# Performance work log

Measured on AMD Instinct MI355X. Metric: run time of the kernel, lower is better.

Reference implementation:

```python
import jax, jax.numpy as jnp
import numpy as np

B, D, H = 4096, 64, 512  # batch, event dim, MLP hidden


def _net(z, t, W1, b1, W2, b2, W3, b3):
    # z: [..., D]; t: scalar, broadcast as a time feature column
    tcol = jnp.broadcast_to(t, z.shape[:-1] + (1,))
    x = jnp.concatenate([z, tcol], axis=-1)            # [..., D+1]
    h = jnp.tanh(x @ W1 + b1)                          # [..., H]
    h = jnp.tanh(h @ W2 + b2)                          # [..., H]
    return h @ W3 + b3                                 # [..., D]


def setup_inputs() -> dict:
    key = jax.random.key(0)
    ks = jax.random.split(key, 6)
    s_in = 1.0 / np.sqrt(D + 1)
    s_h = 1.0 / np.sqrt(H)
    return {
        "z": jax.random.normal(ks[0], (B, D), dtype=jnp.float32),
        "log_pz": jnp.zeros((B, 1), dtype=jnp.float32),
        "t": jax.random.uniform(ks[1], (1,), dtype=jnp.float32),
        "W1": jax.random.normal(ks[2], (D + 1, H), dtype=jnp.float32) * s_in,
        "b1": jnp.zeros((H,), dtype=jnp.float32),
        "W2": jax.random.normal(ks[3], (H, H), dtype=jnp.float32) * s_h,
        "b2": jnp.zeros((H,), dtype=jnp.float32),
        "W3": jax.random.normal(ks[4], (H, D), dtype=jnp.float32) * s_h,
        "b3": jnp.zeros((D,), dtype=jnp.float32),
    }


def reference(z, log_pz, t, W1, b1, W2, b2, W3, b3):
    tval = t[0]
    # velocity field v = net(z, t), batched
    v = _net(z, tval, W1, b1, W2, b2, W3, b3)          # [B, D]
    # exact Jacobian trace: replaces the torch per-dim autograd.grad loop
    # with a fully vectorized per-sample forward-mode Jacobian.
    f_single = lambda zi: _net(zi, tval, W1, b1, W2, b2, W3, b3)  # [D] -> [D]
    jac = jax.vmap(jax.jacfwd(f_single))(z)            # [B, D, D]
    dlogp_dt = -jnp.trace(jac, axis1=1, axis2=2)[:, None]  # [B, 1]
    return (v, dlogp_dt)
```

## Files before the change

### kernel.cpp

```cpp
#include <hip/hip_runtime.h>
#include <hip/hip_bf16.h>

#define BB 4096
#define DD 64
#define HH 512

typedef short short8 __attribute__((ext_vector_type(8)));
typedef float f32x4  __attribute__((ext_vector_type(4)));
typedef __hip_bfloat16 bf16;

__device__ __forceinline__ float tanh_fast(float x) {
    float e = __expf(2.0f * x);
    return 1.0f - __fdividef(2.0f, 1.0f + e);
}

__device__ __forceinline__ void st_swz(bf16* base, int row, int col, int rs, float v) {
    base[row * rs + ((((col >> 3) ^ (row & 7))) << 3) + (col & 7)] = __float2bfloat16(v);
}

#define GLD1(dst, addr)                                                      \
  asm volatile("global_load_dwordx4 %0, %1, off" : "=&v"(dst) : "v"(addr))

#define GLD2(e0, e1, addr)                                                   \
  asm volatile("global_load_dwordx4 %0, %2, off\n\t"                         \
               "global_load_dwordx4 %1, %2, off offset:1024"                 \
               : "=&v"(e0), "=&v"(e1) : "v"(addr))

#define GLD4(e0, e1, e2, e3, addr)                                           \
  asm volatile("global_load_dwordx4 %0, %4, off\n\t"                         \
               "global_load_dwordx4 %1, %4, off offset:1024\n\t"             \
               "global_load_dwordx4 %2, %4, off offset:2048\n\t"             \
               "global_load_dwordx4 %3, %4, off offset:3072"                 \
               : "=&v"(e0), "=&v"(e1), "=&v"(e2), "=&v"(e3) : "v"(addr))

#define WAITV(n)                                                             \
  do { asm volatile("s_waitcnt vmcnt(" #n ")" ::: "memory");                 \
       __builtin_amdgcn_sched_barrier(0); } while (0)

#define LGKMBAR()                                                            \
  do { asm volatile("s_waitcnt lgkmcnt(0)" ::: "memory");                    \
       __builtin_amdgcn_s_barrier();                                         \
       __builtin_amdgcn_sched_barrier(0); } while (0)

__global__ __launch_bounds__(256) void prep_kernel(
    const float* __restrict__ t, const float* __restrict__ W1,
    const float* __restrict__ b1, const float* __restrict__ W2,
    const float* __restrict__ W3, const float* __restrict__ b3,
    bf16* __restrict__ W1p, bf16* __restrict__ W2p, bf16* __restrict__ W3p,
    bf16* __restrict__ Pp, float* __restrict__ b1eff, float* __restrict__ out)
{
    const int tid  = threadIdx.x;
    const int bx   = blockIdx.x;
    const int lane = tid & 63;
    const int r    = lane & 15;
    const int kq   = lane >> 4;

    if (bx < 160) {
        int T = bx * 4 + (tid >> 6);
        const float* src;
        bf16* dst;
        int stride;
        if (T < 64) {
            int w = T >> 2, s = (T >> 1) & 1, f = T & 1;
            src = W1 + (size_t)(s * 32 + kq * 8) * HH + (w * 2 + f) * 16 + r;
            stride = HH;
            dst = W1p + (size_t)T * 512 + lane * 8;
        } else if (T < 576) {
            int tt = T - 64;
            int cw = tt >> 4, s = tt & 15;
            src = W2 + (size_t)(s * 32 + kq * 8) * HH + cw * 16 + r;
            stride = HH;
            dst = W2p + (size_t)tt * 512 + lane * 8;
        } else {
            int tt = T - 576;
            int q = tt >> 2, f = tt & 3;
            src = W3 + (size_t)(q * 32 + kq * 8) * DD + f * 16 + r;
            stride = DD;
            dst = W3p + (size_t)tt * 512 + lane * 8;
        }
        short8 v;
#pragma unroll
        for (int j = 0; j < 8; ++j)
            v[j] = (short)__bfloat16_as_ushort(__float2bfloat16(src[(size_t)j * stride]));
        *(short8*)dst = v;
    } else if (bx < 288) {
        int pt = (bx - 160) * 4 + (tid >> 6);
        int cw = pt >> 4, s = pt & 15;
        int k  = cw * 16 + r;
        int j0 = s * 32 + kq * 8;
        float acc[8] = {};
        const float* w3row = W3 + (size_t)k * DD;
        for (int d = 0; d < DD; ++d) {
            float w3 = w3row[d];
            const float4* w1p4 = (const float4*)(W1 + (size_t)d * HH + j0);
            float4 x = w1p4[0], y = w1p4[1];
            acc[0] += x.x * w3; acc[1] += x.y * w3;
            acc[2] += x.z * w3; acc[3] += x.w * w3;
            acc[4] += y.x * w3; acc[5] += y.y * w3;
            acc[6] += y.z * w3; acc[7] += y.w * w3;
        }
        short8 v;
#pragma unroll
        for (int j = 0; j < 8; ++j)
            v[j] = (short)__bfloat16_as_ushort(
                __float2bfloat16(acc[j] * W2[(size_t)(j0 + j) * HH + k]));
        *(short8*)(Pp + (size_t)pt * 512 + lane * 8) = v;
    } else if (bx == 288) {
        float tv = t[0];
        b1eff[tid]       = b1[tid]       + tv * W1[(size_t)64 * HH + tid];
        b1eff[tid + 256] = b1[tid + 256] + tv * W1[(size_t)64 * HH + tid + 256];
    } else {
        int idx = (bx - 289) * 1024 + tid * 4;
        if (idx < BB * DD) {
            int col = idx & 63;
            *(float4*)(out + idx) =
                make_float4(b3[col], b3[col + 1], b3[col + 2], b3[col + 3]);
        } else {
            *(float4*)(out + idx) = make_float4(0.f, 0.f, 0.f, 0.f);
        }
    }
}

__global__ __launch_bounds__(1024, 2) void fused_rows(
    const float* __restrict__ z, const bf16* __restrict__ W1p,
    const bf16* __restrict__ W2p, const bf16* __restrict__ W3p,
    const bf16* __restrict__ Pp, const float* __restrict__ b1eff,
    const float* __restrict__ b2,
    float* __restrict__ outV, float* __restrict__ outTr)
{
    __shared__ alignas(16) char smem[88064];
    bf16* zt   = (bf16*)smem;
    bf16* h1   = (bf16*)(smem + 4096);
    bf16* at   = (bf16*)(smem + 36864);
    bf16* h2   = (bf16*)(smem + 69632);
    float* trp = (float*)(smem + 86016);
    float* vp  = (float*)smem;

    const int tid  = threadIdx.x;
    const int wid  = tid >> 6;
    const int lane = tid & 63;
    const int r    = lane & 15;
    const int kq   = lane >> 4;
    const int rx   = r & 7;
    const int laneE = lane * 8;
    const int rt   = blockIdx.x >> 1;
    const int ch   = blockIdx.x & 1;
    const int bm   = rt * 32;

    float bias1[2];
#pragma unroll
    for (int f = 0; f < 2; ++f) bias1[f] = b1eff[wid * 32 + f * 16 + r];
    float bias2 = b2[ch * 256 + wid * 16 + r];
    asm volatile("" :: "v"(bias1[0]), "v"(bias1[1]), "v"(bias2));

    {
        int i = tid * 2;
        int row = i >> 6, col = i & 63;
        float2 v = *(const float2*)(z + (size_t)(bm + row) * DD + col);
        st_swz(zt, row, col,     64, v.x);
        st_swz(zt, row, col + 1, 64, v.y);
    }

    short8 q0, q1, q2, q3, p0, p1;
    const bf16* Wb1 = W1p + (size_t)wid * 2048 + laneE;
    GLD2(q0, q1, Wb1);
    GLD2(p0, p1, Wb1 + 1024);
    LGKMBAR();

    f32x4 acc1[2][2] = {};
    WAITV(2);
#pragma unroll
    for (int g = 0; g < 2; ++g) {
        short8 av = *(const short8*)(zt + (g * 16 + r) * 64 + ((kq ^ rx) << 3));
        acc1[g][0] = __builtin_amdgcn_mfma_f32_16x16x32_bf16(av, q0, acc1[g][0], 0, 0, 0);
        acc1[g][1] = __builtin_amdgcn_mfma_f32_16x16x32_bf16(av, q1, acc1[g][1], 0, 0, 0);
    }
    WAITV(0);
#pragma unroll
    for (int g = 0; g < 2; ++g) {
        short8 av = *(const short8*)(zt + (g * 16 + r) * 64 + (((4 + kq) ^ rx) << 3));
        acc1[g][0] = __builtin_amdgcn_mfma_f32_16x16x32_bf16(av, p0, acc1[g][0], 0, 0, 0);
        acc1[g][1] = __builtin_amdgcn_mfma_f32_16x16x32_bf16(av, p1, acc1[g][1], 0, 0, 0);
    }
    short8 rbW[4], rbP[4];
    const bf16* Wb2 = W2p + (size_t)(ch * 16 + wid) * 8192 + laneE;
    const bf16* WbE = Pp  + (size_t)(ch * 16 + wid) * 8192 + laneE;
    GLD1(rbW[0], Wb2);        GLD1(rbP[0], WbE);
    GLD1(rbW[1], Wb2 + 512);  GLD1(rbP[1], WbE + 512);
    GLD1(rbW[2], Wb2 + 1024); GLD1(rbP[2], WbE + 1024);
#pragma unroll
    for (int g = 0; g < 2; ++g)
#pragma unroll
        for (int f = 0; f < 2; ++f) {
            int col = wid * 32 + f * 16 + r;
#pragma unroll
            for (int v = 0; v < 4; ++v) {
                int row = g * 16 + kq * 4 + v;
                float h = tanh_fast(acc1[g][f][v] + bias1[f]);
                st_swz(h1, row, col, 512, h);
                st_swz(at, row, col, 512, fmaf(-h, h, 1.0f));
            }
        }
    LGKMBAR();

    f32x4 acc2[2] = {};
    f32x4 accE[2] = {};
#pragma unroll
    for (int s = 0; s < 16; ++s) {
        int co = (((s * 4 + kq) ^ rx) << 3);
        short8 a1v[2], aav[2];
#pragma unroll
        for (int g = 0; g < 2; ++g) {
            a1v[g] = *(const short8*)(h1 + (g * 16 + r) * 512 + co);
            aav[g] = *(const short8*)(at + (g * 16 + r) * 512 + co);
        }
        if (s + 3 < 16) {
            GLD1(rbW[(s + 3) & 3], Wb2 + (s + 3) * 512);
            GLD1(rbP[(s + 3) & 3], WbE + (s + 3) * 512);
            WAITV(6);
        } else if (s + 2 < 16) { WAITV(4); }
        else if (s + 1 < 16)   { WAITV(2); }
        else                   { WAITV(0); }
#pragma unroll
        for (int g = 0; g < 2; ++g) {
            acc2[g] = __builtin_amdgcn_mfma_f32_16x16x32_bf16(a1v[g], rbW[s & 3], acc2[g], 0, 0, 0);
            accE[g] = __builtin_amdgcn_mfma_f32_16x16x32_bf16(aav[g], rbP[s & 3], accE[g], 0, 0, 0);
        }
    }
    f32x4 bsq[2];
    {
        int colL = wid * 16 + r;
#pragma unroll
        for (int g = 0; g < 2; ++g)
#pragma unroll
            for (int v = 0; v < 4; ++v) {
                int row = g * 16 + kq * 4 + v;
                float h = tanh_fast(acc2[g][v] + bias2);
                st_swz(h2, row, colL, 256, h);
                bsq[g][v] = fmaf(-h, h, 1.0f);
            }
        const int kw = wid & 7;
        const bf16* Wb3 = W3p + (size_t)(ch * 8 + kw) * 2048 + laneE;
        GLD4(q0, q1, q2, q3, Wb3);
#pragma unroll
        for (int g = 0; g < 2; ++g)
#pragma unroll
            for (int v = 0; v < 4; ++v) {
                float p = accE[g][v] * bsq[g][v];
                p += __shfl_xor(p, 1);
                p += __shfl_xor(p, 2);
                p += __shfl_xor(p, 4);
                p += __shfl_xor(p, 8);
                if (r == 0) trp[wid * 32 + g * 16 + kq * 4 + v] = p;
            }
    }
    LGKMBAR();

    {
        const int kw = wid & 7, rp = wid >> 3;
        f32x4 c0 = {}, c1 = {}, c2 = {}, c3 = {};
        short8 av = *(const short8*)(h2 + (rp * 16 + r) * 256 + (((kw * 4 + kq) ^ rx) << 3));
        WAITV(0);
        c0 = __builtin_amdgcn_mfma_f32_16x16x32_bf16(av, q0, c0, 0, 0, 0);
        c1 = __builtin_amdgcn_mfma_f32_16x16x32_bf16(av, q1, c1, 0, 0, 0);
        c2 = __builtin_amdgcn_mfma_f32_16x16x32_bf16(av, q2, c2, 0, 0, 0);
        c3 = __builtin_amdgcn_mfma_f32_16x16x32_bf16(av, q3, c3, 0, 0, 0);
#pragma unroll
        for (int v = 0; v < 4; ++v) {
            int row = rp * 16 + kq * 4 + v;
            vp[kw * 2048 + row * 64 + 0 * 16 + r] = c0[v];
            vp[kw * 2048 + row * 64 + 1 * 16 + r] = c1[v];
            vp[kw * 2048 + row * 64 + 2 * 16 + r] = c2[v];
            vp[kw * 2048 + row * 64 + 3 * 16 + r] = c3[v];
        }
    }
    LGKMBAR();

#pragma unroll
    for (int it = 0; it < 2; ++it) {
        int i = it * 1024 + tid;
        int row = i >> 6, col = i & 63;
        float s = 0.f;
#pragma unroll
        for (int kw = 0; kw < 8; ++kw) s += vp[kw * 2048 + i];
        atomicAdd(outV + (size_t)(bm + row) * DD + col, s);
    }
    if (tid < 32) {
        float s = 0.f;
#pragma unroll
        for (int w = 0; w < 16; ++w) s += trp[w * 32 + tid];
        atomicAdd(outTr + bm + tid, -s);
    }
}

extern "C" void kernel_launch(void* const* d_in, const int* in_sizes, int n_in,
                              void* d_out, int out_size, void* d_ws, size_t ws_size,
                              hipStream_t stream)
{
    const float* z  = (const float*)d_in[0];
    const float* t  = (const float*)d_in[2];
    const float* W1 = (const float*)d_in[3];
    const float* b1 = (const float*)d_in[4];
    const float* W2 = (const float*)d_in[5];
    const float* b2 = (const float*)d_in[6];
    const float* W3 = (const float*)d_in[7];
    const float* b3 = (const float*)d_in[8];
    float* out = (float*)d_out;
    float* out_tr = out + (size_t)BB * DD;

    char* w = (char*)d_ws;
    auto alloc = [&](size_t bytes) {
        char* p = w;
        w += (bytes + 255) & ~(size_t)255;
        return p;
    };
    bf16* W1p   = (bf16*)alloc((size_t)64  * 512 * 2);
    bf16* W2p   = (bf16*)alloc((size_t)512 * 512 * 2);
    bf16* W3p   = (bf16*)alloc((size_t)64  * 512 * 2);
    bf16* Pp    = (bf16*)alloc((size_t)512 * 512 * 2);
    float* b1eff = (float*)alloc((size_t)HH * 4);

    prep_kernel<<<549, 256, 0, stream>>>(t, W1, b1, W2, W3, b3,
                                         W1p, W2p, W3p, Pp, b1eff, out);
    fused_rows<<<128 * 2, 1024, 0, stream>>>(z, W1p, W2p, W3p, Pp,
                                             b1eff, b2, out, out_tr);
}
```

Measured before the change: 26.57 us.

## Replace output atomics with partial buffers and reduce kernel; pack bf16 LDS stores

The main kernel now writes each half's partial V and trace results to workspace buffers with plain stores instead of atomically adding into a pre-initialized output. A third kernel sums the two halves and adds b3, so the prep kernel no longer has to initialize the output. LDS stores for z, h1, a and h2 are packed into 32-bit bf16 pairs using lane shuffles. The W2/P prefetch pipeline is deepened from 4 to 5 stages, and the vp scratch gets a padded row stride of 68 to reduce bank conflicts. In exchange there is an extra kernel launch and extra global traffic for the partial buffers.

```diff
diff --git a/kernel.cpp b/kernel.cpp
--- a/kernel.cpp
+++ b/kernel.cpp
@@ -14,8 +14,14 @@
     return 1.0f - __fdividef(2.0f, 1.0f + e);
 }
 
-__device__ __forceinline__ void st_swz(bf16* base, int row, int col, int rs, float v) {
-    base[row * rs + ((((col >> 3) ^ (row & 7))) << 3) + (col & 7)] = __float2bfloat16(v);
+__device__ __forceinline__ unsigned pk2(float lo, float hi) {
+    return (unsigned)__bfloat16_as_ushort(__float2bfloat16(lo)) |
+           ((unsigned)__bfloat16_as_ushort(__float2bfloat16(hi)) << 16);
+}
+
+__device__ __forceinline__ void st_swz32(bf16* base, int row, int col, int rs, unsigned v) {
+    int e = row * rs + ((((col >> 3) ^ (row & 7))) << 3) + (col & 7);
+    *(unsigned*)(base + e) = v;
 }
 
 #define GLD1(dst, addr)                                                      \
@@ -45,9 +51,9 @@
 __global__ __launch_bounds__(256) void prep_kernel(
     const float* __restrict__ t, const float* __restrict__ W1,
     const float* __restrict__ b1, const float* __restrict__ W2,
-    const float* __restrict__ W3, const float* __restrict__ b3,
+    const float* __restrict__ W3,
     bf16* __restrict__ W1p, bf16* __restrict__ W2p, bf16* __restrict__ W3p,
-    bf16* __restrict__ Pp, float* __restrict__ b1eff, float* __restrict__ out)
+    bf16* __restrict__ Pp, float* __restrict__ b1eff)
 {
     const int tid  = threadIdx.x;
     const int bx   = blockIdx.x;
@@ -105,19 +111,10 @@
             v[j] = (short)__bfloat16_as_ushort(
                 __float2bfloat16(acc[j] * W2[(size_t)(j0 + j) * HH + k]));
         *(short8*)(Pp + (size_t)pt * 512 + lane * 8) = v;
-    } else if (bx == 288) {
+    } else {
         float tv = t[0];
         b1eff[tid]       = b1[tid]       + tv * W1[(size_t)64 * HH + tid];
         b1eff[tid + 256] = b1[tid + 256] + tv * W1[(size_t)64 * HH + tid + 256];
-    } else {
-        int idx = (bx - 289) * 1024 + tid * 4;
-        if (idx < BB * DD) {
-            int col = idx & 63;
-            *(float4*)(out + idx) =
-                make_float4(b3[col], b3[col + 1], b3[col + 2], b3[col + 3]);
-        } else {
-            *(float4*)(out + idx) = make_float4(0.f, 0.f, 0.f, 0.f);
-        }
     }
 }
 
@@ -126,7 +123,7 @@
     const bf16* __restrict__ W2p, const bf16* __restrict__ W3p,
     const bf16* __restrict__ Pp, const float* __restrict__ b1eff,
     const float* __restrict__ b2,
-    float* __restrict__ outV, float* __restrict__ outTr)
+    float* __restrict__ vpart, float* __restrict__ tpart)
 {
     __shared__ alignas(16) char smem[88064];
     bf16* zt   = (bf16*)smem;
@@ -146,6 +143,8 @@
     const int rt   = blockIdx.x >> 1;
     const int ch   = blockIdx.x & 1;
     const int bm   = rt * 32;
+    float* myV = vpart + (size_t)ch * (BB * DD);
+    float* myT = tpart + (size_t)ch * BB;
 
     float bias1[2];
 #pragma unroll
@@ -157,8 +156,7 @@
         int i = tid * 2;
         int row = i >> 6, col = i & 63;
         float2 v = *(const float2*)(z + (size_t)(bm + row) * DD + col);
-        st_swz(zt, row, col,     64, v.x);
-        st_swz(zt, row, col + 1, 64, v.y);
+        st_swz32(zt, row, col, 64, pk2(v.x, v.y));
     }
 
     short8 q0, q1, q2, q3, p0, p1;
@@ -182,12 +180,13 @@
         acc1[g][0] = __builtin_amdgcn_mfma_f32_16x16x32_bf16(av, p0, acc1[g][0], 0, 0, 0);
         acc1[g][1] = __builtin_amdgcn_mfma_f32_16x16x32_bf16(av, p1, acc1[g][1], 0, 0, 0);
     }
-    short8 rbW[4], rbP[4];
+    short8 rbW[5], rbP[5];
     const bf16* Wb2 = W2p + (size_t)(ch * 16 + wid) * 8192 + laneE;
     const bf16* WbE = Pp  + (size_t)(ch * 16 + wid) * 8192 + laneE;
     GLD1(rbW[0], Wb2);        GLD1(rbP[0], WbE);
     GLD1(rbW[1], Wb2 + 512);  GLD1(rbP[1], WbE + 512);
     GLD1(rbW[2], Wb2 + 1024); GLD1(rbP[2], WbE + 1024);
+    GLD1(rbW[3], Wb2 + 1536); GLD1(rbP[3], WbE + 1536);
 #pragma unroll
     for (int g = 0; g < 2; ++g)
 #pragma unroll
@@ -197,8 +196,13 @@
             for (int v = 0; v < 4; ++v) {
                 int row = g * 16 + kq * 4 + v;
                 float h = tanh_fast(acc1[g][f][v] + bias1[f]);
-                st_swz(h1, row, col, 512, h);
-                st_swz(at, row, col, 512, fmaf(-h, h, 1.0f));
+                float a = fmaf(-h, h, 1.0f);
+                float ho = __shfl_xor(h, 1);
+                float ao = __shfl_xor(a, 1);
+                if (!(r & 1)) {
+                    st_swz32(h1, row, col, 512, pk2(h, ho));
+                    st_swz32(at, row, col, 512, pk2(a, ao));
+                }
             }
         }
     LGKMBAR();
@@ -214,17 +218,18 @@
             a1v[g] = *(const short8*)(h1 + (g * 16 + r) * 512 + co);
             aav[g] = *(const short8*)(at + (g * 16 + r) * 512 + co);
         }
-        if (s + 3 < 16) {
-            GLD1(rbW[(s + 3) & 3], Wb2 + (s + 3) * 512);
-            GLD1(rbP[(s + 3) & 3], WbE + (s + 3) * 512);
-            WAITV(6);
-        } else if (s + 2 < 16) { WAITV(4); }
+        if (s + 4 < 16) {
+            GLD1(rbW[(s + 4) % 5], Wb2 + (s + 4) * 512);
+            GLD1(rbP[(s + 4) % 5], WbE + (s + 4) * 512);
+            WAITV(8);
+        } else if (s + 3 < 16) { WAITV(6); }
+        else if (s + 2 < 16)   { WAITV(4); }
         else if (s + 1 < 16)   { WAITV(2); }
         else                   { WAITV(0); }
 #pragma unroll
         for (int g = 0; g < 2; ++g) {
-            acc2[g] = __builtin_amdgcn_mfma_f32_16x16x32_bf16(a1v[g], rbW[s & 3], acc2[g], 0, 0, 0);
-            accE[g] = __builtin_amdgcn_mfma_f32_16x16x32_bf16(aav[g], rbP[s & 3], accE[g], 0, 0, 0);
+            acc2[g] = __builtin_amdgcn_mfma_f32_16x16x32_bf16(a1v[g], rbW[s % 5], acc2[g], 0, 0, 0);
+            accE[g] = __builtin_amdgcn_mfma_f32_16x16x32_bf16(aav[g], rbP[s % 5], accE[g], 0, 0, 0);
         }
     }
     f32x4 bsq[2];
@@ -236,8 +241,9 @@
             for (int v = 0; v < 4; ++v) {
                 int row = g * 16 + kq * 4 + v;
                 float h = tanh_fast(acc2[g][v] + bias2);
-                st_swz(h2, row, colL, 256, h);
                 bsq[g][v] = fmaf(-h, h, 1.0f);
+                float ho = __shfl_xor(h, 1);
+                if (!(r & 1)) st_swz32(h2, row, colL, 256, pk2(h, ho));
             }
         const int kw = wid & 7;
         const bf16* Wb3 = W3p + (size_t)(ch * 8 + kw) * 2048 + laneE;
@@ -268,10 +274,10 @@
 #pragma unroll
         for (int v = 0; v < 4; ++v) {
             int row = rp * 16 + kq * 4 + v;
-            vp[kw * 2048 + row * 64 + 0 * 16 + r] = c0[v];
-            vp[kw * 2048 + row * 64 + 1 * 16 + r] = c1[v];
-            vp[kw * 2048 + row * 64 + 2 * 16 + r] = c2[v];
-            vp[kw * 2048 + row * 64 + 3 * 16 + r] = c3[v];
+            vp[kw * 2176 + row * 68 + 0 * 16 + r] = c0[v];
+            vp[kw * 2176 + row * 68 + 1 * 16 + r] = c1[v];
+            vp[kw * 2176 + row * 68 + 2 * 16 + r] = c2[v];
+            vp[kw * 2176 + row * 68 + 3 * 16 + r] = c3[v];
         }
     }
     LGKMBAR();
@@ -282,14 +288,35 @@
         int row = i >> 6, col = i & 63;
         float s = 0.f;
 #pragma unroll
-        for (int kw = 0; kw < 8; ++kw) s += vp[kw * 2048 + i];
-        atomicAdd(outV + (size_t)(bm + row) * DD + col, s);
+        for (int kw = 0; kw < 8; ++kw) s += vp[kw * 2176 + row * 68 + col];
+        myV[(size_t)(bm + row) * DD + col] = s;
     }
     if (tid < 32) {
         float s = 0.f;
 #pragma unroll
         for (int w = 0; w < 16; ++w) s += trp[w * 32 + tid];
-        atomicAdd(outTr + bm + tid, -s);
+        myT[bm + tid] = -s;
+    }
+}
+
+__global__ __launch_bounds__(256) void reduce_out(
+    const float* __restrict__ vpart, const float* __restrict__ tpart,
+    const float* __restrict__ b3, float* __restrict__ out)
+{
+    int idx = blockIdx.x * 256 + threadIdx.x;
+    if (idx < 65536) {
+        float4 a = ((const float4*)vpart)[idx];
+        float4 b = ((const float4*)(vpart + BB * DD))[idx];
+        float4 c = *(const float4*)(b3 + ((idx * 4) & 63));
+        float4 s = make_float4(a.x + b.x + c.x, a.y + b.y + c.y,
+                               a.z + b.z + c.z, a.w + b.w + c.w);
+        ((float4*)out)[idx] = s;
+    } else {
+        int i = idx - 65536;
+        float4 a = ((const float4*)tpart)[i];
+        float4 b = ((const float4*)(tpart + BB))[i];
+        float4 s = make_float4(a.x + b.x, a.y + b.y, a.z + b.z, a.w + b.w);
+        ((float4*)(out + BB * DD))[i] = s;
     }
 }
 
@@ -306,7 +333,6 @@
     const float* W3 = (const float*)d_in[7];
     const float* b3 = (const float*)d_in[8];
     float* out = (float*)d_out;
-    float* out_tr = out + (size_t)BB * DD;
 
     char* w = (char*)d_ws;
     auto alloc = [&](size_t bytes) {
@@ -319,9 +345,12 @@
     bf16* W3p   = (bf16*)alloc((size_t)64  * 512 * 2);
     bf16* Pp    = (bf16*)alloc((size_t)512 * 512 * 2);
     float* b1eff = (float*)alloc((size_t)HH * 4);
-
-    prep_kernel<<<549, 256, 0, stream>>>(t, W1, b1, W2, W3, b3,
-                                         W1p, W2p, W3p, Pp, b1eff, out);
+    float* vpart = (float*)alloc((size_t)2 * BB * DD * 4);
+    float* tpart = (float*)alloc((size_t)2 * BB * 4);
+
+    prep_kernel<<<289, 256, 0, stream>>>(t, W1, b1, W2, W3,
+                                         W1p, W2p, W3p, Pp, b1eff);
     fused_rows<<<128 * 2, 1024, 0, stream>>>(z, W1p, W2p, W3p, Pp,
-                                             b1eff, b2, out, out_tr);
-}
+                                             b1eff, b2, vpart, tpart);
+    reduce_out<<<260, 256, 0, stream>>>(vpart, tpart, b3, out);
+}
```

After: 29.47 us. 1.11x slower.
